# Kernel tuning notes

Measured on AMD Instinct MI355X. Metric: run time of the kernel, lower is better.

The kernel has to match this reference:

```python
import jax, jax.numpy as jnp
import numpy as np

B, T, S, H = 4, 128, 512, 512


def setup_inputs() -> dict:
    key = jax.random.key(0)
    k1, k2, k3, k4, k5, k6, k7 = jax.random.split(key, 7)
    query = jax.random.normal(k1, (B, T, H), dtype=jnp.float32)
    encoder_outputs = jax.random.normal(k2, (B, S, H), dtype=jnp.float32)
    src_lengths = jax.random.randint(k3, (B,), 1, S + 1)
    src_lengths = src_lengths.at[0].set(S)  # torch code assumes max(len) == S
    scale = 1.0 / np.sqrt(H)
    W_h = jax.random.normal(k4, (H, H), dtype=jnp.float32) * scale
    W_s = jax.random.normal(k5, (H, H), dtype=jnp.float32) * scale
    v = jax.random.normal(k6, (H,), dtype=jnp.float32) * scale
    W_out = jax.random.normal(k7, (2 * H, H), dtype=jnp.float32) * scale
    return {"query": query, "encoder_outputs": encoder_outputs,
            "src_lengths": src_lengths, "W_h": W_h, "W_s": W_s,
            "v": v, "W_out": W_out}


def reference(query, encoder_outputs, src_lengths, W_h, W_s, v, W_out):
    # Project once, then broadcast (same math as torch's Linear on expanded tensors)
    pq = jnp.einsum('bth,hk->btk', query, W_s)            # (B,T,H) : W_s applied to query
    pe = jnp.einsum('bsh,hk->bsk', encoder_outputs, W_h)  # (B,S,H) : W_h applied to encoder
    # score(h_i, s_j) = v^T tanh(W_s q + W_h e)
    score = jnp.einsum('btsh,h->bts', jnp.tanh(pq[:, :, None, :] + pe[:, None, :, :]), v)  # (B,T,S)
    mask = (jnp.arange(score.shape[-1]) [None, :] < src_lengths[:, None])[:, None, :]  # (B,1,S)
    score = jnp.where(mask, score, -jnp.inf)
    alignment = jax.nn.softmax(score, axis=-1)            # (B,T,S)
    context = jnp.einsum('bts,bsh->bth', alignment, encoder_outputs)  # (B,T,H)
    attn_out = jnp.tanh(jnp.concatenate([context, query], axis=-1) @ W_out)  # (B,T,H)
    return attn_out
```

## Files before the change

kernel.cpp:

```cpp
#include <hip/hip_runtime.h>
#include <math.h>

#define HD 512
#define BB 4
#define TT 128
#define SS 512

typedef __attribute__((ext_vector_type(8))) short short8;
typedef __attribute__((ext_vector_type(4))) float floatx4;
typedef _Float16 half2_t __attribute__((ext_vector_type(2)));
typedef unsigned short ushort_t;
typedef unsigned int uint_t;

__device__ __forceinline__ float tanh_e(float x) {
    float t = __builtin_amdgcn_rcpf(__expf(2.f * x) + 1.f);
    return fmaf(-2.f, t, 1.f);
}
__device__ __forceinline__ ushort_t f2bf(float x) {
    unsigned int u = __float_as_uint(x);
    u += 0x7fffu + ((u >> 16) & 1u);
    return (ushort_t)(u >> 16);
}

__global__ __launch_bounds__(256) void wtrans_kernel(
    const float* __restrict__ Ws, const float* __restrict__ Wh,
    const float* __restrict__ Wo, const float* __restrict__ query,
    const float* __restrict__ enc,
    ushort_t* __restrict__ Ts, ushort_t* __restrict__ Th, ushort_t* __restrict__ To,
    ushort_t* __restrict__ cq, ushort_t* __restrict__ encB)
{
    const int bid = blockIdx.x;
    const int tid = threadIdx.x;
    if (bid < 128) {
        const float* src; ushort_t* dst; int K, l;
        if (bid < 32)      { src = Ws; dst = Ts; K = 512;  l = bid;      }
        else if (bid < 64) { src = Wh; dst = Th; K = 512;  l = bid - 32; }
        else               { src = Wo; dst = To; K = 1024; l = bid - 64; }
        const int ktiles = K >> 7;
        const int tk = l & (ktiles - 1), tn = l / ktiles;
        const int k0 = tk * 128, n0 = tn * 64;

        __shared__ ushort_t tile[64][136];

        const int lr  = tid >> 4;
        const int lc4 = (tid & 15) * 4;
        #pragma unroll
        for (int p = 0; p < 8; ++p) {
            const int row = p * 16 + lr;
            float4 s = *(const float4*)(src + (size_t)(k0 + row) * HD + n0 + lc4);
            tile[lc4 + 0][row] = f2bf(s.x);
            tile[lc4 + 1][row] = f2bf(s.y);
            tile[lc4 + 2][row] = f2bf(s.z);
            tile[lc4 + 3][row] = f2bf(s.w);
        }
        __syncthreads();
        const int n = tid >> 2, kc = (tid & 3) * 32;
        #pragma unroll
        for (int j = 0; j < 4; ++j) {
            uint4 o = *(const uint4*)&tile[n][kc + j * 8];
            *(uint4*)&dst[(size_t)(n0 + n) * K + k0 + kc + j * 8] = o;
        }
    } else if (bid < 256) {
        const int idx = ((bid - 128) * 256 + tid) * 8;
        const int m = idx >> 9, h = idx & 511;
        float4 q0 = *(const float4*)(query + (size_t)m * HD + h);
        float4 q1 = *(const float4*)(query + (size_t)m * HD + h + 4);
        uint4 o;
        o.x = (uint_t)f2bf(q0.x) | ((uint_t)f2bf(q0.y) << 16);
        o.y = (uint_t)f2bf(q0.z) | ((uint_t)f2bf(q0.w) << 16);
        o.z = (uint_t)f2bf(q1.x) | ((uint_t)f2bf(q1.y) << 16);
        o.w = (uint_t)f2bf(q1.z) | ((uint_t)f2bf(q1.w) << 16);
        *(uint4*)&cq[(size_t)m * 1024 + 512 + h] = o;
    } else {
        const size_t idx = ((size_t)(bid - 256) * 256 + tid) * 8;
        float4 e0 = *(const float4*)(enc + idx);
        float4 e1 = *(const float4*)(enc + idx + 4);
        uint4 o;
        o.x = (uint_t)f2bf(e0.x) | ((uint_t)f2bf(e0.y) << 16);
        o.y = (uint_t)f2bf(e0.z) | ((uint_t)f2bf(e0.w) << 16);
        o.z = (uint_t)f2bf(e1.x) | ((uint_t)f2bf(e1.y) << 16);
        o.w = (uint_t)f2bf(e1.z) | ((uint_t)f2bf(e1.w) << 16);
        *(uint4*)&encB[idx] = o;
    }
}

#define LDP 40
__global__ __launch_bounds__(256) void proj_kernel(
    const ushort_t* __restrict__ cq, const ushort_t* __restrict__ encB,
    const ushort_t* __restrict__ WTs, const ushort_t* __restrict__ WTh,
    const ushort_t* __restrict__ WTo, const float* __restrict__ v,
    float2* __restrict__ tqa, _Float16* __restrict__ peT,
    _Float16* __restrict__ encWo, float* __restrict__ qWob)
{
    const int bm = blockIdx.x;
    const int bn = blockIdx.y;
    int type; const ushort_t* A; int lda; const ushort_t* B; int ldb; int m0;
    if (bm < 8)       { type = 0; A = cq + 512; lda = 1024; B = WTs;       ldb = 512;  m0 = bm * 64;        }
    else if (bm < 40) { type = 1; A = encB;     lda = 512;  B = WTh;       ldb = 512;  m0 = (bm - 8) * 64;  }
    else if (bm < 72) { type = 2; A = encB;     lda = 512;  B = WTo;       ldb = 1024; m0 = (bm - 40) * 64; }
    else              { type = 3; A = cq + 512; lda = 1024; B = WTo + 512; ldb = 1024; m0 = (bm - 72) * 64; }
    const int n0 = bn * 64;

    __shared__ ushort_t As[64 * LDP];
    __shared__ ushort_t Bs[64 * LDP];

    const int tid = threadIdx.x;
    const int lane = tid & 63, w = tid >> 6;
    const int quad = lane >> 4, lrow = lane & 15;
    const int mw = (w & 1) * 32, nw = (w >> 1) * 32;

    const int ar = tid >> 2;
    const int ac = (tid & 3) * 8;

    floatx4 zero = {0.f, 0.f, 0.f, 0.f};
    floatx4 acc[2][2] = {{zero, zero}, {zero, zero}};

    uint4 ald = *(const uint4*)&A[(size_t)(m0 + ar) * lda + ac];
    uint4 bld = *(const uint4*)&B[(size_t)(n0 + ar) * ldb + ac];

    for (int k0 = 0; k0 < HD; k0 += 32) {
        __syncthreads();
        *(uint4*)&As[ar * LDP + ac] = ald;
        *(uint4*)&Bs[ar * LDP + ac] = bld;
        __syncthreads();
        if (k0 + 32 < HD) {
            ald = *(const uint4*)&A[(size_t)(m0 + ar) * lda + k0 + 32 + ac];
            bld = *(const uint4*)&B[(size_t)(n0 + ar) * ldb + k0 + 32 + ac];
        }
        short8 af[2], bf[2];
        #pragma unroll
        for (int i = 0; i < 2; ++i)
            af[i] = *(const short8*)&As[(mw + i * 16 + lrow) * LDP + quad * 8];
        #pragma unroll
        for (int j = 0; j < 2; ++j)
            bf[j] = *(const short8*)&Bs[(nw + j * 16 + lrow) * LDP + quad * 8];
        #pragma unroll
        for (int i = 0; i < 2; ++i)
            #pragma unroll
            for (int j = 0; j < 2; ++j)
                acc[i][j] = __builtin_amdgcn_mfma_f32_16x16x32_bf16(af[i], bf[j], acc[i][j], 0, 0, 0);
    }

    if (type == 0) {
        #pragma unroll
        for (int j = 0; j < 2; ++j) {
            const int col = n0 + nw + j * 16 + lrow;
            const float vj = v[col];
            #pragma unroll
            for (int i = 0; i < 2; ++i)
                #pragma unroll
                for (int r = 0; r < 4; ++r) {
                    const int row = m0 + mw + i * 16 + quad * 4 + r;
                    float tq = tanh_e(acc[i][j][r]);
                    float2 o; o.x = tq; o.y = vj * tq;
                    tqa[(size_t)row * HD + col] = o;
                }
        }
    } else if (type == 1) {
        #pragma unroll
        for (int i = 0; i < 2; ++i)
            #pragma unroll
            for (int j = 0; j < 2; ++j) {
                const int gm = m0 + mw + i * 16 + quad * 4;
                const int b = gm >> 9, s = gm & 511;
                const int col = n0 + nw + j * 16 + lrow;
                _Float16 t0 = (_Float16)tanh_e(acc[i][j][0]);
                _Float16 t1 = (_Float16)tanh_e(acc[i][j][1]);
                _Float16 t2 = (_Float16)tanh_e(acc[i][j][2]);
                _Float16 t3 = (_Float16)tanh_e(acc[i][j][3]);
                ushort4 o;
                o.x = *(ushort_t*)&t0; o.y = *(ushort_t*)&t1;
                o.z = *(ushort_t*)&t2; o.w = *(ushort_t*)&t3;
                *(ushort4*)((ushort_t*)peT + ((size_t)b * HD + col) * SS + s) = o;
            }
    } else if (type == 2) {
        #pragma unroll
        for (int i = 0; i < 2; ++i)
            #pragma unroll
            for (int j = 0; j < 2; ++j) {
                const int col = n0 + nw + j * 16 + lrow;
                #pragma unroll
                for (int r = 0; r < 4; ++r) {
                    const int gm = m0 + mw + i * 16 + quad * 4 + r;
                    encWo[(size_t)gm * HD + col] = (_Float16)acc[i][j][r];
                }
            }
    } else {
        #pragma unroll
        for (int i = 0; i < 2; ++i)
            #pragma unroll
            for (int j = 0; j < 2; ++j) {
                const int col = n0 + nw + j * 16 + lrow;
                #pragma unroll
                for (int r = 0; r < 4; ++r) {
                    const int gm = m0 + mw + i * 16 + quad * 4 + r;
                    qWob[(size_t)gm * HD + col] = acc[i][j][r];
                }
            }
    }
}

__global__ __launch_bounds__(1024, 4) void fused_kernel(
    const float2* __restrict__ tqa, const _Float16* __restrict__ peT,
    const float* __restrict__ vv, const _Float16* __restrict__ encWo,
    const float* __restrict__ qWob, const int* __restrict__ lens,
    float* __restrict__ out)
{
    const int bt0 = blockIdx.x * 2;
    const int b = bt0 >> 7;
    const int tid = threadIdx.x;
    const int lane = tid & 63, wid = tid >> 6;
    const int len = lens[b];

    __shared__ uint4  s_tab[2][HD];
    __shared__ float  s_part[16][2][SS];
    __shared__ float  s_sc[2][SS];
    __shared__ uint_t s_al2[SS][2];
    __shared__ float  s_red[32];

    {
        const int t_loc = tid >> 9, h = tid & 511;
        float2 q = tqa[(size_t)(bt0 + t_loc) * HD + h];
        float vh = vv[h];
        _Float16 tqh = (_Float16)q.x, vvh = (_Float16)vh, vth = (_Float16)q.y;
        uint_t ta = *(ushort_t*)&tqh, tb = *(ushort_t*)&vvh, tc = *(ushort_t*)&vth;
        uint4 e4; e4.x = ta | (ta << 16); e4.y = tb | (tb << 16); e4.z = tc | (tc << 16); e4.w = 0;
        s_tab[t_loc][h] = e4;
    }
    __syncthreads();

    const int sg = tid & 63;
    const int hq = (tid >> 6) & 7, sub = tid >> 9;
    const int s0 = sg * 8;
    const int hbase = hq * 64 + sub * 32;
    float p0[8] = {0.f,0.f,0.f,0.f,0.f,0.f,0.f,0.f};
    float p1[8] = {0.f,0.f,0.f,0.f,0.f,0.f,0.f,0.f};
    if (s0 < len) {
        const ushort_t* colp = (const ushort_t*)peT + ((size_t)b * HD + hbase) * SS + s0;
        const uint4* tp0 = &s_tab[0][hbase];
        const uint4* tp1 = &s_tab[1][hbase];
        half2_t one2; one2[0] = (_Float16)1.f; one2[1] = (_Float16)1.f;
        #pragma unroll 2
        for (int i = 0; i < 16; ++i) {
            uint4 pA = *(const uint4*)(colp);
            uint4 pB = *(const uint4*)(colp + SS);
            colp += 2 * SS;
            uint4 cA0 = tp0[2 * i], cB0 = tp0[2 * i + 1];
            uint4 cA1 = tp1[2 * i], cB1 = tp1[2 * i + 1];
            half2_t teA0 = *(half2_t*)&pA.x, teA1 = *(half2_t*)&pA.y;
            half2_t teA2 = *(half2_t*)&pA.z, teA3 = *(half2_t*)&pA.w;
            half2_t teB0 = *(half2_t*)&pB.x, teB1 = *(half2_t*)&pB.y;
            half2_t teB2 = *(half2_t*)&pB.z, teB3 = *(half2_t*)&pB.w;
            {
                half2_t tqA = *(half2_t*)&cA0.x, vA = *(half2_t*)&cA0.y, vtA = *(half2_t*)&cA0.z;
                half2_t tqB = *(half2_t*)&cB0.x, vB = *(half2_t*)&cB0.y, vtB = *(half2_t*)&cB0.z;
                half2_t dA0 = tqA * teA0 + one2, dA1 = tqA * teA1 + one2;
                half2_t dA2 = tqA * teA2 + one2, dA3 = tqA * teA3 + one2;
                half2_t dB0 = tqB * teB0 + one2, dB1 = tqB * teB1 + one2;
                half2_t dB2 = tqB * teB2 + one2, dB3 = tqB * teB3 + one2;
                half2_t mA0 = vA * teA0 + vtA, mA1 = vA * teA1 + vtA;
                half2_t mA2 = vA * teA2 + vtA, mA3 = vA * teA3 + vtA;
                half2_t mB0 = vB * teB0 + vtB, mB1 = vB * teB1 + vtB;
                half2_t mB2 = vB * teB2 + vtB, mB3 = vB * teB3 + vtB;
                half2_t n0h = mA0 * dB0 + mB0 * dA0, n1h = mA1 * dB1 + mB1 * dA1;
                half2_t n2h = mA2 * dB2 + mB2 * dA2, n3h = mA3 * dB3 + mB3 * dA3;
                half2_t d0h = dA0 * dB0, d1h = dA1 * dB1;
                half2_t d2h = dA2 * dB2, d3h = dA3 * dB3;
                p0[0] = fmaf((float)n0h[0], __builtin_amdgcn_rcpf((float)d0h[0]), p0[0]);
                p0[1] = fmaf((float)n0h[1], __builtin_amdgcn_rcpf((float)d0h[1]), p0[1]);
                p0[2] = fmaf((float)n1h[0], __builtin_amdgcn_rcpf((float)d1h[0]), p0[2]);
                p0[3] = fmaf((float)n1h[1], __builtin_amdgcn_rcpf((float)d1h[1]), p0[3]);
                p0[4] = fmaf((float)n2h[0], __builtin_amdgcn_rcpf((float)d2h[0]), p0[4]);
                p0[5] = fmaf((float)n2h[1], __builtin_amdgcn_rcpf((float)d2h[1]), p0[5]);
                p0[6] = fmaf((float)n3h[0], __builtin_amdgcn_rcpf((float)d3h[0]), p0[6]);
                p0[7] = fmaf((float)n3h[1], __builtin_amdgcn_rcpf((float)d3h[1]), p0[7]);
            }
            {
                half2_t tqA = *(half2_t*)&cA1.x, vA = *(half2_t*)&cA1.y, vtA = *(half2_t*)&cA1.z;
                half2_t tqB = *(half2_t*)&cB1.x, vB = *(half2_t*)&cB1.y, vtB = *(half2_t*)&cB1.z;
                half2_t dA0 = tqA * teA0 + one2, dA1 = tqA * teA1 + one2;
                half2_t dA2 = tqA * teA2 + one2, dA3 = tqA * teA3 + one2;
                half2_t dB0 = tqB * teB0 + one2, dB1 = tqB * teB1 + one2;
                half2_t dB2 = tqB * teB2 + one2, dB3 = tqB * teB3 + one2;
                half2_t mA0 = vA * teA0 + vtA, mA1 = vA * teA1 + vtA;
                half2_t mA2 = vA * teA2 + vtA, mA3 = vA * teA3 + vtA;
                half2_t mB0 = vB * teB0 + vtB, mB1 = vB * teB1 + vtB;
                half2_t mB2 = vB * teB2 + vtB, mB3 = vB * teB3 + vtB;
                half2_t n0h = mA0 * dB0 + mB0 * dA0, n1h = mA1 * dB1 + mB1 * dA1;
                half2_t n2h = mA2 * dB2 + mB2 * dA2, n3h = mA3 * dB3 + mB3 * dA3;
                half2_t d0h = dA0 * dB0, d1h = dA1 * dB1;
                half2_t d2h = dA2 * dB2, d3h = dA3 * dB3;
                p1[0] = fmaf((float)n0h[0], __builtin_amdgcn_rcpf((float)d0h[0]), p1[0]);
                p1[1] = fmaf((float)n0h[1], __builtin_amdgcn_rcpf((float)d0h[1]), p1[1]);
                p1[2] = fmaf((float)n1h[0], __builtin_amdgcn_rcpf((float)d1h[0]), p1[2]);
                p1[3] = fmaf((float)n1h[1], __builtin_amdgcn_rcpf((float)d1h[1]), p1[3]);
                p1[4] = fmaf((float)n2h[0], __builtin_amdgcn_rcpf((float)d2h[0]), p1[4]);
                p1[5] = fmaf((float)n2h[1], __builtin_amdgcn_rcpf((float)d2h[1]), p1[5]);
                p1[6] = fmaf((float)n3h[0], __builtin_amdgcn_rcpf((float)d3h[0]), p1[6]);
                p1[7] = fmaf((float)n3h[1], __builtin_amdgcn_rcpf((float)d3h[1]), p1[7]);
            }
        }
    }
    {
        float4 w0; w0.x = p0[0]; w0.y = p0[1]; w0.z = p0[2]; w0.w = p0[3];
        float4 w1; w1.x = p0[4]; w1.y = p0[5]; w1.z = p0[6]; w1.w = p0[7];
        *(float4*)&s_part[wid][0][s0]     = w0;
        *(float4*)&s_part[wid][0][s0 + 4] = w1;
        float4 w2; w2.x = p1[0]; w2.y = p1[1]; w2.z = p1[2]; w2.w = p1[3];
        float4 w3; w3.x = p1[4]; w3.y = p1[5]; w3.z = p1[6]; w3.w = p1[7];
        *(float4*)&s_part[wid][1][s0]     = w2;
        *(float4*)&s_part[wid][1][s0 + 4] = w3;
    }
    __syncthreads();
    {
        const int t_loc = tid >> 9, s = tid & 511;
        float acc = 0.f;
        #pragma unroll
        for (int q = 0; q < 16; ++q) acc += s_part[q][t_loc][s];
        s_sc[t_loc][s] = (s < len) ? acc : -INFINITY;
    }
    __syncthreads();

    {
        const int t_loc = tid >> 9;
        float sc = s_sc[t_loc][tid & 511];
        float m = sc;
        #pragma unroll
        for (int off = 32; off; off >>= 1) m = fmaxf(m, __shfl_xor(m, off, 64));
        if (lane == 0) s_red[wid] = m;
        __syncthreads();
        const int rb = (t_loc << 3);
        m = s_red[rb];
        #pragma unroll
        for (int i2 = 1; i2 < 8; ++i2) m = fmaxf(m, s_red[rb + i2]);

        float e = __expf(sc - m);
        float sum = e;
        #pragma unroll
        for (int off = 32; off; off >>= 1) sum += __shfl_xor(sum, off, 64);
        if (lane == 0) s_red[16 + wid] = sum;
        __syncthreads();
        float total = s_red[16 + rb];
        #pragma unroll
        for (int i2 = 1; i2 < 8; ++i2) total += s_red[16 + rb + i2];
        float a = e * __builtin_amdgcn_rcpf(total);
        _Float16 ah = (_Float16)a;
        uint_t ap = *(ushort_t*)&ah;
        s_al2[tid & 511][t_loc] = ap | (ap << 16);
    }
    __syncthreads();

    const int ng = tid & 127, sq = tid >> 7;
    const int n0 = ng * 4;
    const int sbeg = sq * 64;
    float fo0[4] = {0.f, 0.f, 0.f, 0.f};
    float fo1[4] = {0.f, 0.f, 0.f, 0.f};
    {
        const ushort_t* ew = (const ushort_t*)encWo + ((size_t)b * SS + sbeg) * HD + n0;
        const int rem = (len > sbeg) ? ((len - sbeg < 64) ? len - sbeg : 64) : 0;
        const int schunks = (rem + 7) >> 3;
        for (int c = 0; c < schunks; ++c) {
            half2_t a01_0, a23_0, a01_1, a23_1;
            a01_0[0] = (_Float16)0.f; a01_0[1] = (_Float16)0.f;
            a23_0 = a01_0; a01_1 = a01_0; a23_1 = a01_0;
            const ushort_t* ewc = ew + (size_t)(c * 8) * HD;
            #pragma unroll
            for (int k = 0; k < 8; ++k) {
                uint2 wv = *(const uint2*)(ewc + (size_t)k * HD);
                uint2 av = *(const uint2*)&s_al2[sbeg + c * 8 + k][0];
                half2_t w01 = *(half2_t*)&wv.x, w23 = *(half2_t*)&wv.y;
                half2_t al0 = *(half2_t*)&av.x, al1 = *(half2_t*)&av.y;
                a01_0 = al0 * w01 + a01_0; a23_0 = al0 * w23 + a23_0;
                a01_1 = al1 * w01 + a01_1; a23_1 = al1 * w23 + a23_1;
            }
            fo0[0] += (float)a01_0[0]; fo0[1] += (float)a01_0[1];
            fo0[2] += (float)a23_0[0]; fo0[3] += (float)a23_0[1];
            fo1[0] += (float)a01_1[0]; fo1[1] += (float)a01_1[1];
            fo1[2] += (float)a23_1[0]; fo1[3] += (float)a23_1[1];
        }
    }
    __syncthreads();
    {
        float4 w0; w0.x = fo0[0]; w0.y = fo0[1]; w0.z = fo0[2]; w0.w = fo0[3];
        float4 w1; w1.x = fo1[0]; w1.y = fo1[1]; w1.z = fo1[2]; w1.w = fo1[3];
        *(float4*)&s_part[sq][0][n0] = w0;
        *(float4*)&s_part[sq][1][n0] = w1;
    }
    __syncthreads();
    {
        const int t_loc = tid >> 9, n = tid & 511;
        float acc = 0.f;
        #pragma unroll
        for (int q = 0; q < 8; ++q) acc += s_part[q][t_loc][n];
        acc += qWob[(size_t)(bt0 + t_loc) * HD + n];
        out[(size_t)(bt0 + t_loc) * HD + n] = tanh_e(acc);
    }
}

extern "C" void kernel_launch(void* const* d_in, const int* in_sizes, int n_in,
                              void* d_out, int out_size, void* d_ws, size_t ws_size,
                              hipStream_t stream) {
    (void)in_sizes; (void)n_in; (void)out_size; (void)ws_size;
    const float* query = (const float*)d_in[0];
    const float* enc   = (const float*)d_in[1];
    const int*   lens  = (const int*)d_in[2];
    const float* W_h   = (const float*)d_in[3];
    const float* W_s   = (const float*)d_in[4];
    const float* v     = (const float*)d_in[5];
    const float* W_out = (const float*)d_in[6];
    float* out = (float*)d_out;

    ushort_t* WTs   = (ushort_t*)d_ws;
    ushort_t* WTh   = WTs + (size_t)HD * HD;
    ushort_t* WTo   = WTh + (size_t)HD * HD;
    ushort_t* encB  = WTo + (size_t)HD * 2 * HD;
    float2*   tqa   = (float2*)(encB + (size_t)BB * SS * HD);
    _Float16* peT   = (_Float16*)(tqa + (size_t)BB * TT * HD);
    _Float16* encWo = peT + (size_t)BB * HD * SS;
    float*    qWob  = (float*)(encWo + (size_t)BB * SS * HD);
    ushort_t* cq    = (ushort_t*)(qWob + (size_t)BB * TT * HD);

    wtrans_kernel<<<dim3(768), 256, 0, stream>>>(W_s, W_h, W_out, query, enc,
                                                 WTs, WTh, WTo, cq, encB);
    proj_kernel<<<dim3(80, 8), 256, 0, stream>>>(cq, encB, WTs, WTh, WTo, v,
                                                 tqa, peT, encWo, qWob);
    fused_kernel<<<dim3(BB * TT / 2), 1024, 0, stream>>>(tqa, peT, v, encWo, qWob, lens, out);
}
```

Before: 112.5 us.

## Merge three kernels into one cooperative persistent kernel with grid syncs

Replaces the three launches (weight/input conversion, projection GEMMs, fused score/softmax/context) with a single cooperative kernel of 256 blocks of 1024 threads. Each block runs four virtual 256-thread sub-blocks in the first two phases, and grid-wide syncs separate the phases. This removes launch overhead and inter-kernel gaps. In exchange, the GEMM phase keeps four sub-blocks in lockstep through shared __syncthreads, the grid syncs have their own cost, and the old launches remain as a fallback if the cooperative launch fails.

```diff
diff --git a/kernel.cpp b/kernel.cpp
--- a/kernel.cpp
+++ b/kernel.cpp
@@ -1,10 +1,14 @@
 #include <hip/hip_runtime.h>
+#include <hip/hip_cooperative_groups.h>
 #include <math.h>
+
+namespace cg = cooperative_groups;
 
 #define HD 512
 #define BB 4
 #define TT 128
 #define SS 512
+#define LDP 40
 
 typedef __attribute__((ext_vector_type(8))) short short8;
 typedef __attribute__((ext_vector_type(4))) float floatx4;
@@ -84,7 +88,6 @@
     }
 }
 
-#define LDP 40
 __global__ __launch_bounds__(256) void proj_kernel(
     const ushort_t* __restrict__ cq, const ushort_t* __restrict__ encB,
     const ushort_t* __restrict__ WTs, const ushort_t* __restrict__ WTh,
@@ -397,6 +400,387 @@
     }
 }
 
+__global__ __launch_bounds__(1024, 4) void mega_kernel(
+    const float* __restrict__ query, const float* __restrict__ enc,
+    const int* __restrict__ lens,
+    const float* __restrict__ W_h, const float* __restrict__ W_s,
+    const float* __restrict__ vvec, const float* __restrict__ W_out,
+    ushort_t* __restrict__ WTs, ushort_t* __restrict__ WTh, ushort_t* __restrict__ WTo,
+    ushort_t* __restrict__ cq, ushort_t* __restrict__ encB,
+    float2* __restrict__ tqa, _Float16* __restrict__ peT,
+    _Float16* __restrict__ encWo, float* __restrict__ qWob,
+    float* __restrict__ out)
+{
+    cg::grid_group gg = cg::this_grid();
+    const int tid = threadIdx.x;
+    const int bid = blockIdx.x;
+    __shared__ __align__(16) char smem[90240];
+
+    {
+        const int slot = tid >> 8, vtid = tid & 255;
+        const int vb = bid * 4 + slot;
+        const float* srcW = nullptr; ushort_t* dstW = nullptr; int KW = 512;
+        int k0 = 0, n0 = 0;
+        if (vb < 128) {
+            int l;
+            if (vb < 32)      { srcW = W_s;   dstW = WTs; KW = 512;  l = vb; }
+            else if (vb < 64) { srcW = W_h;   dstW = WTh; KW = 512;  l = vb - 32; }
+            else              { srcW = W_out; dstW = WTo; KW = 1024; l = vb - 64; }
+            const int ktiles = KW >> 7;
+            k0 = (l & (ktiles - 1)) * 128;
+            n0 = (l / ktiles) * 64;
+            ushort_t* tile = (ushort_t*)(smem + slot * 17408);
+            const int lr = vtid >> 4, lc4 = (vtid & 15) * 4;
+            #pragma unroll
+            for (int p = 0; p < 8; ++p) {
+                const int row = p * 16 + lr;
+                float4 s4 = *(const float4*)(srcW + (size_t)(k0 + row) * HD + n0 + lc4);
+                tile[(lc4 + 0) * 136 + row] = f2bf(s4.x);
+                tile[(lc4 + 1) * 136 + row] = f2bf(s4.y);
+                tile[(lc4 + 2) * 136 + row] = f2bf(s4.z);
+                tile[(lc4 + 3) * 136 + row] = f2bf(s4.w);
+            }
+        } else if (vb < 256) {
+            const int idx = ((vb - 128) * 256 + vtid) * 8;
+            const int m = idx >> 9, h = idx & 511;
+            float4 q0 = *(const float4*)(query + (size_t)m * HD + h);
+            float4 q1 = *(const float4*)(query + (size_t)m * HD + h + 4);
+            uint4 o;
+            o.x = (uint_t)f2bf(q0.x) | ((uint_t)f2bf(q0.y) << 16);
+            o.y = (uint_t)f2bf(q0.z) | ((uint_t)f2bf(q0.w) << 16);
+            o.z = (uint_t)f2bf(q1.x) | ((uint_t)f2bf(q1.y) << 16);
+            o.w = (uint_t)f2bf(q1.z) | ((uint_t)f2bf(q1.w) << 16);
+            *(uint4*)&cq[(size_t)m * 1024 + 512 + h] = o;
+        } else if (vb < 768) {
+            const size_t idx = ((size_t)(vb - 256) * 256 + vtid) * 8;
+            float4 e0 = *(const float4*)(enc + idx);
+            float4 e1 = *(const float4*)(enc + idx + 4);
+            uint4 o;
+            o.x = (uint_t)f2bf(e0.x) | ((uint_t)f2bf(e0.y) << 16);
+            o.y = (uint_t)f2bf(e0.z) | ((uint_t)f2bf(e0.w) << 16);
+            o.z = (uint_t)f2bf(e1.x) | ((uint_t)f2bf(e1.y) << 16);
+            o.w = (uint_t)f2bf(e1.z) | ((uint_t)f2bf(e1.w) << 16);
+            *(uint4*)&encB[idx] = o;
+        }
+        __syncthreads();
+        if (vb < 128) {
+            ushort_t* tile = (ushort_t*)(smem + slot * 17408);
+            const int n = vtid >> 2, kc = (vtid & 3) * 32;
+            #pragma unroll
+            for (int j = 0; j < 4; ++j) {
+                uint4 o = *(const uint4*)&tile[n * 136 + kc + j * 8];
+                *(uint4*)&dstW[(size_t)(n0 + n) * KW + k0 + kc + j * 8] = o;
+            }
+        }
+    }
+    __threadfence();
+    gg.sync();
+
+    {
+        const int slot = tid >> 8, vtid = tid & 255;
+        const int vb = bid * 4 + slot;
+        const bool active = (vb < 640);
+        const int va = active ? vb : 0;
+        const int bm = va >> 3, bn = va & 7;
+        int type; const ushort_t* A; int lda; const ushort_t* B; int ldb; int m0;
+        if (bm < 8)       { type = 0; A = cq + 512; lda = 1024; B = WTs;       ldb = 512;  m0 = bm * 64; }
+        else if (bm < 40) { type = 1; A = encB;     lda = 512;  B = WTh;       ldb = 512;  m0 = (bm - 8) * 64; }
+        else if (bm < 72) { type = 2; A = encB;     lda = 512;  B = WTo;       ldb = 1024; m0 = (bm - 40) * 64; }
+        else              { type = 3; A = cq + 512; lda = 1024; B = WTo + 512; ldb = 1024; m0 = (bm - 72) * 64; }
+        const int n0 = bn * 64;
+
+        ushort_t* As = (ushort_t*)(smem + slot * 10240);
+        ushort_t* Bs = As + 64 * LDP;
+
+        const int lane = vtid & 63, w = vtid >> 6;
+        const int quad = lane >> 4, lrow = lane & 15;
+        const int mw = (w & 1) * 32, nw = (w >> 1) * 32;
+        const int ar = vtid >> 2, ac = (vtid & 3) * 8;
+
+        floatx4 zero = {0.f, 0.f, 0.f, 0.f};
+        floatx4 acc[2][2] = {{zero, zero}, {zero, zero}};
+
+        uint4 ald = *(const uint4*)&A[(size_t)(m0 + ar) * lda + ac];
+        uint4 bld = *(const uint4*)&B[(size_t)(n0 + ar) * ldb + ac];
+
+        for (int k0 = 0; k0 < HD; k0 += 32) {
+            __syncthreads();
+            *(uint4*)&As[ar * LDP + ac] = ald;
+            *(uint4*)&Bs[ar * LDP + ac] = bld;
+            __syncthreads();
+            if (k0 + 32 < HD) {
+                ald = *(const uint4*)&A[(size_t)(m0 + ar) * lda + k0 + 32 + ac];
+                bld = *(const uint4*)&B[(size_t)(n0 + ar) * ldb + k0 + 32 + ac];
+            }
+            short8 af[2], bf[2];
+            #pragma unroll
+            for (int i = 0; i < 2; ++i)
+                af[i] = *(const short8*)&As[(mw + i * 16 + lrow) * LDP + quad * 8];
+            #pragma unroll
+            for (int j = 0; j < 2; ++j)
+                bf[j] = *(const short8*)&Bs[(nw + j * 16 + lrow) * LDP + quad * 8];
+            #pragma unroll
+            for (int i = 0; i < 2; ++i)
+                #pragma unroll
+                for (int j = 0; j < 2; ++j)
+                    acc[i][j] = __builtin_amdgcn_mfma_f32_16x16x32_bf16(af[i], bf[j], acc[i][j], 0, 0, 0);
+        }
+
+        if (active) {
+            if (type == 0) {
+                #pragma unroll
+                for (int j = 0; j < 2; ++j) {
+                    const int col = n0 + nw + j * 16 + lrow;
+                    const float vj = vvec[col];
+                    #pragma unroll
+                    for (int i = 0; i < 2; ++i)
+                        #pragma unroll
+                        for (int r = 0; r < 4; ++r) {
+                            const int row = m0 + mw + i * 16 + quad * 4 + r;
+                            float tq = tanh_e(acc[i][j][r]);
+                            float2 o; o.x = tq; o.y = vj * tq;
+                            tqa[(size_t)row * HD + col] = o;
+                        }
+                }
+            } else if (type == 1) {
+                #pragma unroll
+                for (int i = 0; i < 2; ++i)
+                    #pragma unroll
+                    for (int j = 0; j < 2; ++j) {
+                        const int gm = m0 + mw + i * 16 + quad * 4;
+                        const int b = gm >> 9, s = gm & 511;
+                        const int col = n0 + nw + j * 16 + lrow;
+                        _Float16 t0 = (_Float16)tanh_e(acc[i][j][0]);
+                        _Float16 t1 = (_Float16)tanh_e(acc[i][j][1]);
+                        _Float16 t2 = (_Float16)tanh_e(acc[i][j][2]);
+                        _Float16 t3 = (_Float16)tanh_e(acc[i][j][3]);
+                        ushort4 o;
+                        o.x = *(ushort_t*)&t0; o.y = *(ushort_t*)&t1;
+                        o.z = *(ushort_t*)&t2; o.w = *(ushort_t*)&t3;
+                        *(ushort4*)((ushort_t*)peT + ((size_t)b * HD + col) * SS + s) = o;
+                    }
+            } else if (type == 2) {
+                #pragma unroll
+                for (int i = 0; i < 2; ++i)
+                    #pragma unroll
+                    for (int j = 0; j < 2; ++j) {
+                        const int col = n0 + nw + j * 16 + lrow;
+                        #pragma unroll
+                        for (int r = 0; r < 4; ++r) {
+                            const int gm = m0 + mw + i * 16 + quad * 4 + r;
+                            encWo[(size_t)gm * HD + col] = (_Float16)acc[i][j][r];
+                        }
+                    }
+            } else {
+                #pragma unroll
+                for (int i = 0; i < 2; ++i)
+                    #pragma unroll
+                    for (int j = 0; j < 2; ++j) {
+                        const int col = n0 + nw + j * 16 + lrow;
+                        #pragma unroll
+                        for (int r = 0; r < 4; ++r) {
+                            const int gm = m0 + mw + i * 16 + quad * 4 + r;
+                            qWob[(size_t)gm * HD + col] = acc[i][j][r];
+                        }
+                    }
+            }
+        }
+    }
+    __threadfence();
+    gg.sync();
+
+    {
+        uint4*  st   = (uint4*)smem;
+        float*  sp   = (float*)(smem + 16384);
+        float*  ssc  = (float*)(smem + 81920);
+        uint_t* sal  = (uint_t*)(smem + 86016);
+        float*  sred = (float*)(smem + 90112);
+
+        const int bt0 = bid * 2;
+        const int b = bt0 >> 7;
+        const int lane = tid & 63, wid = tid >> 6;
+        const int len = lens[b];
+
+        {
+            const int t_loc = tid >> 9, h = tid & 511;
+            float2 q = tqa[(size_t)(bt0 + t_loc) * HD + h];
+            float vh = vvec[h];
+            _Float16 tqh = (_Float16)q.x, vvh = (_Float16)vh, vth = (_Float16)q.y;
+            uint_t ta = *(ushort_t*)&tqh, tb = *(ushort_t*)&vvh, tc = *(ushort_t*)&vth;
+            uint4 e4; e4.x = ta | (ta << 16); e4.y = tb | (tb << 16); e4.z = tc | (tc << 16); e4.w = 0;
+            st[t_loc * HD + h] = e4;
+        }
+        __syncthreads();
+
+        const int sg = tid & 63;
+        const int hq = (tid >> 6) & 7, sub = tid >> 9;
+        const int s0 = sg * 8;
+        const int hbase = hq * 64 + sub * 32;
+        float p0[8] = {0.f,0.f,0.f,0.f,0.f,0.f,0.f,0.f};
+        float p1[8] = {0.f,0.f,0.f,0.f,0.f,0.f,0.f,0.f};
+        if (s0 < len) {
+            const ushort_t* colp = (const ushort_t*)peT + ((size_t)b * HD + hbase) * SS + s0;
+            const uint4* tp0 = &st[hbase];
+            const uint4* tp1 = &st[HD + hbase];
+            half2_t one2; one2[0] = (_Float16)1.f; one2[1] = (_Float16)1.f;
+            #pragma unroll 2
+            for (int i = 0; i < 16; ++i) {
+                uint4 pA = *(const uint4*)(colp);
+                uint4 pB = *(const uint4*)(colp + SS);
+                colp += 2 * SS;
+                uint4 cA0 = tp0[2 * i], cB0 = tp0[2 * i + 1];
+                uint4 cA1 = tp1[2 * i], cB1 = tp1[2 * i + 1];
+                half2_t teA0 = *(half2_t*)&pA.x, teA1 = *(half2_t*)&pA.y;
+                half2_t teA2 = *(half2_t*)&pA.z, teA3 = *(half2_t*)&pA.w;
+                half2_t teB0 = *(half2_t*)&pB.x, teB1 = *(half2_t*)&pB.y;
+                half2_t teB2 = *(half2_t*)&pB.z, teB3 = *(half2_t*)&pB.w;
+                {
+                    half2_t tqA = *(half2_t*)&cA0.x, vA = *(half2_t*)&cA0.y, vtA = *(half2_t*)&cA0.z;
+                    half2_t tqB = *(half2_t*)&cB0.x, vB = *(half2_t*)&cB0.y, vtB = *(half2_t*)&cB0.z;
+                    half2_t dA0 = tqA * teA0 + one2, dA1 = tqA * teA1 + one2;
+                    half2_t dA2 = tqA * teA2 + one2, dA3 = tqA * teA3 + one2;
+                    half2_t dB0 = tqB * teB0 + one2, dB1 = tqB * teB1 + one2;
+                    half2_t dB2 = tqB * teB2 + one2, dB3 = tqB * teB3 + one2;
+                    half2_t mA0 = vA * teA0 + vtA, mA1 = vA * teA1 + vtA;
+                    half2_t mA2 = vA * teA2 + vtA, mA3 = vA * teA3 + vtA;
+                    half2_t mB0 = vB * teB0 + vtB, mB1 = vB * teB1 + vtB;
+                    half2_t mB2 = vB * teB2 + vtB, mB3 = vB * teB3 + vtB;
+                    half2_t n0h = mA0 * dB0 + mB0 * dA0, n1h = mA1 * dB1 + mB1 * dA1;
+                    half2_t n2h = mA2 * dB2 + mB2 * dA2, n3h = mA3 * dB3 + mB3 * dA3;
+                    half2_t d0h = dA0 * dB0, d1h = dA1 * dB1;
+                    half2_t d2h = dA2 * dB2, d3h = dA3 * dB3;
+                    p0[0] = fmaf((float)n0h[0], __builtin_amdgcn_rcpf((float)d0h[0]), p0[0]);
+                    p0[1] = fmaf((float)n0h[1], __builtin_amdgcn_rcpf((float)d0h[1]), p0[1]);
+                    p0[2] = fmaf((float)n1h[0], __builtin_amdgcn_rcpf((float)d1h[0]), p0[2]);
+                    p0[3] = fmaf((float)n1h[1], __builtin_amdgcn_rcpf((float)d1h[1]), p0[3]);
+                    p0[4] = fmaf((float)n2h[0], __builtin_amdgcn_rcpf((float)d2h[0]), p0[4]);
+                    p0[5] = fmaf((float)n2h[1], __builtin_amdgcn_rcpf((float)d2h[1]), p0[5]);
+                    p0[6] = fmaf((float)n3h[0], __builtin_amdgcn_rcpf((float)d3h[0]), p0[6]);
+                    p0[7] = fmaf((float)n3h[1], __builtin_amdgcn_rcpf((float)d3h[1]), p0[7]);
+                }
+                {
+                    half2_t tqA = *(half2_t*)&cA1.x, vA = *(half2_t*)&cA1.y, vtA = *(half2_t*)&cA1.z;
+                    half2_t tqB = *(half2_t*)&cB1.x, vB = *(half2_t*)&cB1.y, vtB = *(half2_t*)&cB1.z;
+                    half2_t dA0 = tqA * teA0 + one2, dA1 = tqA * teA1 + one2;
+                    half2_t dA2 = tqA * teA2 + one2, dA3 = tqA * teA3 + one2;
+                    half2_t dB0 = tqB * teB0 + one2, dB1 = tqB * teB1 + one2;
+                    half2_t dB2 = tqB * teB2 + one2, dB3 = tqB * teB3 + one2;
+                    half2_t mA0 = vA * teA0 + vtA, mA1 = vA * teA1 + vtA;
+                    half2_t mA2 = vA * teA2 + vtA, mA3 = vA * teA3 + vtA;
+                    half2_t mB0 = vB * teB0 + vtB, mB1 = vB * teB1 + vtB;
+                    half2_t mB2 = vB * teB2 + vtB, mB3 = vB * teB3 + vtB;
+                    half2_t n0h = mA0 * dB0 + mB0 * dA0, n1h = mA1 * dB1 + mB1 * dA1;
+                    half2_t n2h = mA2 * dB2 + mB2 * dA2, n3h = mA3 * dB3 + mB3 * dA3;
+                    half2_t d0h = dA0 * dB0, d1h = dA1 * dB1;
+                    half2_t d2h = dA2 * dB2, d3h = dA3 * dB3;
+                    p1[0] = fmaf((float)n0h[0], __builtin_amdgcn_rcpf((float)d0h[0]), p1[0]);
+                    p1[1] = fmaf((float)n0h[1], __builtin_amdgcn_rcpf((float)d0h[1]), p1[1]);
+                    p1[2] = fmaf((float)n1h[0], __builtin_amdgcn_rcpf((float)d1h[0]), p1[2]);
+                    p1[3] = fmaf((float)n1h[1], __builtin_amdgcn_rcpf((float)d1h[1]), p1[3]);
+                    p1[4] = fmaf((float)n2h[0], __builtin_amdgcn_rcpf((float)d2h[0]), p1[4]);
+                    p1[5] = fmaf((float)n2h[1], __builtin_amdgcn_rcpf((float)d2h[1]), p1[5]);
+                    p1[6] = fmaf((float)n3h[0], __builtin_amdgcn_rcpf((float)d3h[0]), p1[6]);
+                    p1[7] = fmaf((float)n3h[1], __builtin_amdgcn_rcpf((float)d3h[1]), p1[7]);
+                }
+            }
+        }
+        {
+            float4 w0; w0.x = p0[0]; w0.y = p0[1]; w0.z = p0[2]; w0.w = p0[3];
+            float4 w1; w1.x = p0[4]; w1.y = p0[5]; w1.z = p0[6]; w1.w = p0[7];
+            *(float4*)&sp[(wid * 2 + 0) * SS + s0]     = w0;
+            *(float4*)&sp[(wid * 2 + 0) * SS + s0 + 4] = w1;
+            float4 w2; w2.x = p1[0]; w2.y = p1[1]; w2.z = p1[2]; w2.w = p1[3];
+            float4 w3; w3.x = p1[4]; w3.y = p1[5]; w3.z = p1[6]; w3.w = p1[7];
+            *(float4*)&sp[(wid * 2 + 1) * SS + s0]     = w2;
+            *(float4*)&sp[(wid * 2 + 1) * SS + s0 + 4] = w3;
+        }
+        __syncthreads();
+        {
+            const int t_loc = tid >> 9, s = tid & 511;
+            float acc = 0.f;
+            #pragma unroll
+            for (int q = 0; q < 16; ++q) acc += sp[(q * 2 + t_loc) * SS + s];
+            ssc[t_loc * SS + s] = (s < len) ? acc : -INFINITY;
+        }
+        __syncthreads();
+
+        {
+            const int t_loc = tid >> 9;
+            float sc = ssc[t_loc * SS + (tid & 511)];
+            float m = sc;
+            #pragma unroll
+            for (int off = 32; off; off >>= 1) m = fmaxf(m, __shfl_xor(m, off, 64));
+            if (lane == 0) sred[wid] = m;
+            __syncthreads();
+            const int rb = (t_loc << 3);
+            m = sred[rb];
+            #pragma unroll
+            for (int i2 = 1; i2 < 8; ++i2) m = fmaxf(m, sred[rb + i2]);
+
+            float e = __expf(sc - m);
+            float sum = e;
+            #pragma unroll
+            for (int off = 32; off; off >>= 1) sum += __shfl_xor(sum, off, 64);
+            if (lane == 0) sred[16 + wid] = sum;
+            __syncthreads();
+            float total = sred[16 + rb];
+            #pragma unroll
+            for (int i2 = 1; i2 < 8; ++i2) total += sred[16 + rb + i2];
+            float a = e * __builtin_amdgcn_rcpf(total);
+            _Float16 ah = (_Float16)a;
+            uint_t ap = *(ushort_t*)&ah;
+            sal[(tid & 511) * 2 + t_loc] = ap | (ap << 16);
+        }
+        __syncthreads();
+
+        const int ng = tid & 127, sq = tid >> 7;
+        const int n0 = ng * 4;
+        const int sbeg = sq * 64;
+        float fo0[4] = {0.f, 0.f, 0.f, 0.f};
+        float fo1[4] = {0.f, 0.f, 0.f, 0.f};
+        {
+            const ushort_t* ew = (const ushort_t*)encWo + ((size_t)b * SS + sbeg) * HD + n0;
+            const int rem = (len > sbeg) ? ((len - sbeg < 64) ? len - sbeg : 64) : 0;
+            const int schunks = (rem + 7) >> 3;
+            for (int c = 0; c < schunks; ++c) {
+                half2_t a01_0, a23_0, a01_1, a23_1;
+                a01_0[0] = (_Float16)0.f; a01_0[1] = (_Float16)0.f;
+                a23_0 = a01_0; a01_1 = a01_0; a23_1 = a01_0;
+                const ushort_t* ewc = ew + (size_t)(c * 8) * HD;
+                #pragma unroll
+                for (int k = 0; k < 8; ++k) {
+                    uint2 wv = *(const uint2*)(ewc + (size_t)k * HD);
+                    uint2 av = *(const uint2*)&sal[(sbeg + c * 8 + k) * 2];
+                    half2_t w01 = *(half2_t*)&wv.x, w23 = *(half2_t*)&wv.y;
+                    half2_t al0 = *(half2_t*)&av.x, al1 = *(half2_t*)&av.y;
+                    a01_0 = al0 * w01 + a01_0; a23_0 = al0 * w23 + a23_0;
+                    a01_1 = al1 * w01 + a01_1; a23_1 = al1 * w23 + a23_1;
+                }
+                fo0[0] += (float)a01_0[0]; fo0[1] += (float)a01_0[1];
+                fo0[2] += (float)a23_0[0]; fo0[3] += (float)a23_0[1];
+                fo1[0] += (float)a01_1[0]; fo1[1] += (float)a01_1[1];
+                fo1[2] += (float)a23_1[0]; fo1[3] += (float)a23_1[1];
+            }
+        }
+        __syncthreads();
+        {
+            float4 w0; w0.x = fo0[0]; w0.y = fo0[1]; w0.z = fo0[2]; w0.w = fo0[3];
+            float4 w1; w1.x = fo1[0]; w1.y = fo1[1]; w1.z = fo1[2]; w1.w = fo1[3];
+            *(float4*)&sp[(sq * 2 + 0) * SS + n0] = w0;
+            *(float4*)&sp[(sq * 2 + 1) * SS + n0] = w1;
+        }
+        __syncthreads();
+        {
+            const int t_loc = tid >> 9, n = tid & 511;
+            float acc = 0.f;
+            #pragma unroll
+            for (int q = 0; q < 8; ++q) acc += sp[(q * 2 + t_loc) * SS + n];
+            acc += qWob[(size_t)(bt0 + t_loc) * HD + n];
+            out[(size_t)(bt0 + t_loc) * HD + n] = tanh_e(acc);
+        }
+    }
+}
+
 extern "C" void kernel_launch(void* const* d_in, const int* in_sizes, int n_in,
                               void* d_out, int out_size, void* d_ws, size_t ws_size,
                               hipStream_t stream) {
@@ -420,9 +804,20 @@
     float*    qWob  = (float*)(encWo + (size_t)BB * SS * HD);
     ushort_t* cq    = (ushort_t*)(qWob + (size_t)BB * TT * HD);
 
-    wtrans_kernel<<<dim3(768), 256, 0, stream>>>(W_s, W_h, W_out, query, enc,
-                                                 WTs, WTh, WTo, cq, encB);
-    proj_kernel<<<dim3(80, 8), 256, 0, stream>>>(cq, encB, WTs, WTh, WTo, v,
-                                                 tqa, peT, encWo, qWob);
-    fused_kernel<<<dim3(BB * TT / 2), 1024, 0, stream>>>(tqa, peT, v, encWo, qWob, lens, out);
+    void* args[] = {
+        (void*)&query, (void*)&enc, (void*)&lens,
+        (void*)&W_h, (void*)&W_s, (void*)&v, (void*)&W_out,
+        (void*)&WTs, (void*)&WTh, (void*)&WTo, (void*)&cq, (void*)&encB,
+        (void*)&tqa, (void*)&peT, (void*)&encWo, (void*)&qWob,
+        (void*)&out
+    };
+    hipError_t err = hipLaunchCooperativeKernel(mega_kernel, dim3(256), dim3(1024),
+                                                args, 0, stream);
+    if (err != hipSuccess) {
+        wtrans_kernel<<<dim3(768), 256, 0, stream>>>(W_s, W_h, W_out, query, enc,
+                                                     WTs, WTh, WTo, cq, encB);
+        proj_kernel<<<dim3(80, 8), 256, 0, stream>>>(cq, encB, WTs, WTh, WTo, v,
+                                                     tqa, peT, encWo, qWob);
+        fused_kernel<<<dim3(BB * TT / 2), 1024, 0, stream>>>(tqa, peT, v, encWo, qWob, lens, out);
+    }
 }
```

Measured after the change: 410.9 us. +265.2%, slower.

## Fuse fp32-to-bf16 conversion and weight transpose into projection GEMM loads

Applied to the files above, without the earlier changes.

Drops the separate conversion/transpose kernel and has the projection GEMM read fp32 query, encoder and weights directly. It converts them to bf16 while staging into shared memory, transposing the weights on the fly with strided column loads. This removes a kernel launch and the round trip through workspace buffers. The cost is uncoalesced-ish scalar weight loads (8 rows per thread), twice as many bytes read per tile, and repeated conversion work across blocks.

```diff
diff --git a/kernel.cpp b/kernel.cpp
--- a/kernel.cpp
+++ b/kernel.cpp
@@ -5,6 +5,7 @@
 #define BB 4
 #define TT 128
 #define SS 512
+#define LDP 40
 
 typedef __attribute__((ext_vector_type(8))) short short8;
 typedef __attribute__((ext_vector_type(4))) float floatx4;
@@ -22,83 +23,20 @@
     return (ushort_t)(u >> 16);
 }
 
-__global__ __launch_bounds__(256) void wtrans_kernel(
+__global__ __launch_bounds__(256) void proj_kernel(
+    const float* __restrict__ query, const float* __restrict__ enc,
     const float* __restrict__ Ws, const float* __restrict__ Wh,
-    const float* __restrict__ Wo, const float* __restrict__ query,
-    const float* __restrict__ enc,
-    ushort_t* __restrict__ Ts, ushort_t* __restrict__ Th, ushort_t* __restrict__ To,
-    ushort_t* __restrict__ cq, ushort_t* __restrict__ encB)
-{
-    const int bid = blockIdx.x;
-    const int tid = threadIdx.x;
-    if (bid < 128) {
-        const float* src; ushort_t* dst; int K, l;
-        if (bid < 32)      { src = Ws; dst = Ts; K = 512;  l = bid;      }
-        else if (bid < 64) { src = Wh; dst = Th; K = 512;  l = bid - 32; }
-        else               { src = Wo; dst = To; K = 1024; l = bid - 64; }
-        const int ktiles = K >> 7;
-        const int tk = l & (ktiles - 1), tn = l / ktiles;
-        const int k0 = tk * 128, n0 = tn * 64;
-
-        __shared__ ushort_t tile[64][136];
-
-        const int lr  = tid >> 4;
-        const int lc4 = (tid & 15) * 4;
-        #pragma unroll
-        for (int p = 0; p < 8; ++p) {
-            const int row = p * 16 + lr;
-            float4 s = *(const float4*)(src + (size_t)(k0 + row) * HD + n0 + lc4);
-            tile[lc4 + 0][row] = f2bf(s.x);
-            tile[lc4 + 1][row] = f2bf(s.y);
-            tile[lc4 + 2][row] = f2bf(s.z);
-            tile[lc4 + 3][row] = f2bf(s.w);
-        }
-        __syncthreads();
-        const int n = tid >> 2, kc = (tid & 3) * 32;
-        #pragma unroll
-        for (int j = 0; j < 4; ++j) {
-            uint4 o = *(const uint4*)&tile[n][kc + j * 8];
-            *(uint4*)&dst[(size_t)(n0 + n) * K + k0 + kc + j * 8] = o;
-        }
-    } else if (bid < 256) {
-        const int idx = ((bid - 128) * 256 + tid) * 8;
-        const int m = idx >> 9, h = idx & 511;
-        float4 q0 = *(const float4*)(query + (size_t)m * HD + h);
-        float4 q1 = *(const float4*)(query + (size_t)m * HD + h + 4);
-        uint4 o;
-        o.x = (uint_t)f2bf(q0.x) | ((uint_t)f2bf(q0.y) << 16);
-        o.y = (uint_t)f2bf(q0.z) | ((uint_t)f2bf(q0.w) << 16);
-        o.z = (uint_t)f2bf(q1.x) | ((uint_t)f2bf(q1.y) << 16);
-        o.w = (uint_t)f2bf(q1.z) | ((uint_t)f2bf(q1.w) << 16);
-        *(uint4*)&cq[(size_t)m * 1024 + 512 + h] = o;
-    } else {
-        const size_t idx = ((size_t)(bid - 256) * 256 + tid) * 8;
-        float4 e0 = *(const float4*)(enc + idx);
-        float4 e1 = *(const float4*)(enc + idx + 4);
-        uint4 o;
-        o.x = (uint_t)f2bf(e0.x) | ((uint_t)f2bf(e0.y) << 16);
-        o.y = (uint_t)f2bf(e0.z) | ((uint_t)f2bf(e0.w) << 16);
-        o.z = (uint_t)f2bf(e1.x) | ((uint_t)f2bf(e1.y) << 16);
-        o.w = (uint_t)f2bf(e1.z) | ((uint_t)f2bf(e1.w) << 16);
-        *(uint4*)&encB[idx] = o;
-    }
-}
-
-#define LDP 40
-__global__ __launch_bounds__(256) void proj_kernel(
-    const ushort_t* __restrict__ cq, const ushort_t* __restrict__ encB,
-    const ushort_t* __restrict__ WTs, const ushort_t* __restrict__ WTh,
-    const ushort_t* __restrict__ WTo, const float* __restrict__ v,
+    const float* __restrict__ Wo, const float* __restrict__ v,
     float2* __restrict__ tqa, _Float16* __restrict__ peT,
     _Float16* __restrict__ encWo, float* __restrict__ qWob)
 {
     const int bm = blockIdx.x;
     const int bn = blockIdx.y;
-    int type; const ushort_t* A; int lda; const ushort_t* B; int ldb; int m0;
-    if (bm < 8)       { type = 0; A = cq + 512; lda = 1024; B = WTs;       ldb = 512;  m0 = bm * 64;        }
-    else if (bm < 40) { type = 1; A = encB;     lda = 512;  B = WTh;       ldb = 512;  m0 = (bm - 8) * 64;  }
-    else if (bm < 72) { type = 2; A = encB;     lda = 512;  B = WTo;       ldb = 1024; m0 = (bm - 40) * 64; }
-    else              { type = 3; A = cq + 512; lda = 1024; B = WTo + 512; ldb = 1024; m0 = (bm - 72) * 64; }
+    int type; const float* A; const float* Bw; int m0;
+    if (bm < 8)       { type = 0; A = query; Bw = Ws;                    m0 = bm * 64;        }
+    else if (bm < 40) { type = 1; A = enc;   Bw = Wh;                    m0 = (bm - 8) * 64;  }
+    else if (bm < 72) { type = 2; A = enc;   Bw = Wo;                    m0 = (bm - 40) * 64; }
+    else              { type = 3; A = query; Bw = Wo + (size_t)512 * HD; m0 = (bm - 72) * 64; }
     const int n0 = bn * 64;
 
     __shared__ ushort_t As[64 * LDP];
@@ -109,23 +47,44 @@
     const int quad = lane >> 4, lrow = lane & 15;
     const int mw = (w & 1) * 32, nw = (w >> 1) * 32;
 
-    const int ar = tid >> 2;
-    const int ac = (tid & 3) * 8;
+    const int am = tid >> 2, ak = (tid & 3) * 8;
+    const int bn_ = tid & 63, bkq = tid >> 6;
 
     floatx4 zero = {0.f, 0.f, 0.f, 0.f};
     floatx4 acc[2][2] = {{zero, zero}, {zero, zero}};
 
-    uint4 ald = *(const uint4*)&A[(size_t)(m0 + ar) * lda + ac];
-    uint4 bld = *(const uint4*)&B[(size_t)(n0 + ar) * ldb + ac];
+    float4 a0 = *(const float4*)(A + (size_t)(m0 + am) * HD + ak);
+    float4 a1 = *(const float4*)(A + (size_t)(m0 + am) * HD + ak + 4);
+    float bv0, bv1, bv2, bv3, bv4, bv5, bv6, bv7;
+    {
+        const float* bp = Bw + (size_t)(bkq * 8) * HD + n0 + bn_;
+        bv0 = bp[0 * HD]; bv1 = bp[1 * HD]; bv2 = bp[2 * HD]; bv3 = bp[3 * HD];
+        bv4 = bp[4 * HD]; bv5 = bp[5 * HD]; bv6 = bp[6 * HD]; bv7 = bp[7 * HD];
+    }
 
     for (int k0 = 0; k0 < HD; k0 += 32) {
         __syncthreads();
-        *(uint4*)&As[ar * LDP + ac] = ald;
-        *(uint4*)&Bs[ar * LDP + ac] = bld;
+        {
+            uint4 apk;
+            apk.x = (uint_t)f2bf(a0.x) | ((uint_t)f2bf(a0.y) << 16);
+            apk.y = (uint_t)f2bf(a0.z) | ((uint_t)f2bf(a0.w) << 16);
+            apk.z = (uint_t)f2bf(a1.x) | ((uint_t)f2bf(a1.y) << 16);
+            apk.w = (uint_t)f2bf(a1.z) | ((uint_t)f2bf(a1.w) << 16);
+            *(uint4*)&As[am * LDP + ak] = apk;
+            uint4 bpk;
+            bpk.x = (uint_t)f2bf(bv0) | ((uint_t)f2bf(bv1) << 16);
+            bpk.y = (uint_t)f2bf(bv2) | ((uint_t)f2bf(bv3) << 16);
+            bpk.z = (uint_t)f2bf(bv4) | ((uint_t)f2bf(bv5) << 16);
+            bpk.w = (uint_t)f2bf(bv6) | ((uint_t)f2bf(bv7) << 16);
+            *(uint4*)&Bs[bn_ * LDP + bkq * 8] = bpk;
+        }
         __syncthreads();
         if (k0 + 32 < HD) {
-            ald = *(const uint4*)&A[(size_t)(m0 + ar) * lda + k0 + 32 + ac];
-            bld = *(const uint4*)&B[(size_t)(n0 + ar) * ldb + k0 + 32 + ac];
+            a0 = *(const float4*)(A + (size_t)(m0 + am) * HD + k0 + 32 + ak);
+            a1 = *(const float4*)(A + (size_t)(m0 + am) * HD + k0 + 32 + ak + 4);
+            const float* bp = Bw + (size_t)(k0 + 32 + bkq * 8) * HD + n0 + bn_;
+            bv0 = bp[0 * HD]; bv1 = bp[1 * HD]; bv2 = bp[2 * HD]; bv3 = bp[3 * HD];
+            bv4 = bp[4 * HD]; bv5 = bp[5 * HD]; bv6 = bp[6 * HD]; bv7 = bp[7 * HD];
         }
         short8 af[2], bf[2];
         #pragma unroll
@@ -410,19 +369,12 @@
     const float* W_out = (const float*)d_in[6];
     float* out = (float*)d_out;
 
-    ushort_t* WTs   = (ushort_t*)d_ws;
-    ushort_t* WTh   = WTs + (size_t)HD * HD;
-    ushort_t* WTo   = WTh + (size_t)HD * HD;
-    ushort_t* encB  = WTo + (size_t)HD * 2 * HD;
-    float2*   tqa   = (float2*)(encB + (size_t)BB * SS * HD);
+    float2*   tqa   = (float2*)d_ws;
     _Float16* peT   = (_Float16*)(tqa + (size_t)BB * TT * HD);
     _Float16* encWo = peT + (size_t)BB * HD * SS;
     float*    qWob  = (float*)(encWo + (size_t)BB * SS * HD);
-    ushort_t* cq    = (ushort_t*)(qWob + (size_t)BB * TT * HD);
-
-    wtrans_kernel<<<dim3(768), 256, 0, stream>>>(W_s, W_h, W_out, query, enc,
-                                                 WTs, WTh, WTo, cq, encB);
-    proj_kernel<<<dim3(80, 8), 256, 0, stream>>>(cq, encB, WTs, WTh, WTo, v,
+
+    proj_kernel<<<dim3(80, 8), 256, 0, stream>>>(query, enc, W_s, W_h, W_out, v,
                                                  tqa, peT, encWo, qWob);
     fused_kernel<<<dim3(BB * TT / 2), 1024, 0, stream>>>(tqa, peT, v, encWo, qWob, lens, out);
 }
```

Result: faster. 109.9 us, median of 2 (-2.3%).
